# Optimization experiments

Hardware: AMD Instinct MI355X
Metric: run time of the kernel (lower is better)

## Reference

```python
import jax, jax.numpy as jnp
import numpy as np


def setup_inputs() -> dict:
    key = jax.random.key(0)
    ka, kb = jax.random.split(key)
    a = jax.random.normal(ka, (16384, 3), dtype=jnp.float32)
    b = jax.random.normal(kb, (16384, 3), dtype=jnp.float32)
    return {"a": a, "b": b}


def reference(a, b):
    # Pairwise Euclidean distances via ||a||^2 + ||b||^2 - 2 a.b (avoids [N,M,D] diff tensor).
    a2 = jnp.sum(a * a, axis=-1)            # [N]
    b2 = jnp.sum(b * b, axis=-1)            # [M]
    sq = a2[:, None] + b2[None, :] - 2.0 * jnp.einsum("nd,md->nm", a, b)  # [N,M]
    dist = jnp.sqrt(jnp.maximum(sq, 0.0))
    min_a = jnp.min(dist, axis=1)           # nearest b for each a
    min_b = jnp.min(dist, axis=0)           # nearest a for each b
    return jnp.mean(jnp.concatenate([min_a, min_b]))
```

## Files before the change

### kernel.cpp

```cpp
#include <hip/hip_runtime.h>

typedef unsigned int uint32;
typedef unsigned short ushort16;
typedef __attribute__((ext_vector_type(16))) float f32x16;
typedef __attribute__((ext_vector_type(8)))  short short8;

#define THREADS 256
#define FR 2
#define QB 256
#define JS 8
#define RB 128

__device__ inline ushort16 bf16rn(float x) {
    uint32 u = __float_as_uint(x);
    u += 0x7FFFu + ((u >> 16) & 1u);
    return (ushort16)(u >> 16);
}
__device__ inline float bf2f(ushort16 h) { return __uint_as_float(((uint32)h) << 16); }

__device__ inline void prep_one(const float* __restrict__ P, int np, int i,
                                short8* __restrict__ Qf, short8* __restrict__ Sf,
                                float* __restrict__ a2)
{
    ushort16 qs[16], ss[16];
#pragma unroll
    for (int s = 0; s < 16; ++s) { qs[s] = 0; ss[s] = 0; }
    float w = 0.f;
    if (i < np) {
        float c[3] = {P[3*i], P[3*i+1], P[3*i+2]};
        w = fmaf(c[0], c[0], fmaf(c[1], c[1], c[2]*c[2]));
#pragma unroll
        for (int cc = 0; cc < 3; ++cc) {
            ushort16 h = bf16rn(c[cc]);
            ushort16 m = bf16rn(c[cc] - bf2f(h));
            float bv = -2.f * c[cc];
            ushort16 bh = bf16rn(bv);
            ushort16 bm = bf16rn(bv - bf2f(bh));
            const int b = 4*cc;
            qs[b]=h;  qs[b+1]=h;  qs[b+2]=m;  qs[b+3]=m;
            ss[b]=bh; ss[b+1]=bm; ss[b+2]=bh; ss[b+3]=bm;
        }
        qs[12]=0x3F80; qs[13]=0x3F80; qs[14]=0x3F80;
        ushort16 wh = bf16rn(w);
        float r1 = w - bf2f(wh);
        ushort16 wm = bf16rn(r1);
        ushort16 wl = bf16rn(r1 - bf2f(wm));
        ss[12]=wh; ss[13]=wm; ss[14]=wl;
    } else {
        ss[12] = bf16rn(1e30f);
    }
    a2[i] = w;
    const int row = i & 31, grp = i >> 5;
#pragma unroll
    for (int h = 0; h < 2; ++h) {
        short8 qv, sv;
#pragma unroll
        for (int e = 0; e < 8; ++e) { qv[e] = (short)qs[8*h+e]; sv[e] = (short)ss[8*h+e]; }
        Qf[(size_t)grp*64 + h*32 + row] = qv;
        Sf[(size_t)grp*64 + h*32 + row] = sv;
    }
}

__global__ __launch_bounds__(THREADS) void cd_prep(
    const float* __restrict__ A, int n, int padN,
    const float* __restrict__ B, int m, int padM,
    short8* QfA, short8* SfA, float* a2A,
    short8* QfB, short8* SfB, float* a2B,
    uint32* bits)
{
    const int i = blockIdx.x * THREADS + threadIdx.x;
    if (i < n + m) bits[i] = 0x7F800000u;
    if (i < padN) prep_one(A, n, i, QfA, SfA, a2A);
    if (i < padM) prep_one(B, m, i, QfB, SfB, a2B);
}

__device__ inline float dppmin(float v, int ctrl) {
    float s;
    switch (ctrl) {
        case 0xB1:  s = __int_as_float(__builtin_amdgcn_mov_dpp(__float_as_int(v), 0xB1,  0xf, 0xf, false)); break;
        case 0x4E:  s = __int_as_float(__builtin_amdgcn_mov_dpp(__float_as_int(v), 0x4E,  0xf, 0xf, false)); break;
        case 0x141: s = __int_as_float(__builtin_amdgcn_mov_dpp(__float_as_int(v), 0x141, 0xf, 0xf, false)); break;
        default:    s = __int_as_float(__builtin_amdgcn_mov_dpp(__float_as_int(v), 0x140, 0xf, 0xf, false)); break;
    }
    return fminf(v, s);
}

__global__ __launch_bounds__(THREADS, 4) void cd_mfma(
    const short8* __restrict__ QfA, const short8* __restrict__ SfA,
    const float* __restrict__ a2A, int padN, int n,
    const short8* __restrict__ QfB, const short8* __restrict__ SfB,
    const float* __restrict__ a2B, int padM, int m,
    uint32* __restrict__ bits)
{
    const short8* Qf; const short8* Sf; const float* a2; uint32* outb;
    int nq, padQ, padS;
    if (blockIdx.z == 0) { Qf=QfA; a2=a2A; nq=n; padQ=padN; Sf=SfB; padS=padM; outb=bits;   }
    else                 { Qf=QfB; a2=a2B; nq=m; padQ=padM; Sf=SfA; padS=padN; outb=bits+n; }

    if ((int)(blockIdx.x * QB) >= padQ) return;
    const int ntiles = padS >> 5;
    const int tps = (ntiles + JS - 1) / JS;
    const int t0 = blockIdx.y * tps;
    const int t1 = min(t0 + tps, ntiles);
    if (t0 >= t1) return;

    const int tid = threadIdx.x, lane = tid & 63, wid = tid >> 6;
    const int qbase = blockIdx.x * QB + wid * (FR * 32);

    short8 av[FR];
#pragma unroll
    for (int f = 0; f < FR; ++f)
        av[f] = Qf[(size_t)((qbase >> 5) + f) * 64 + lane];

    float rmin[FR][16];
#pragma unroll
    for (int f = 0; f < FR; ++f)
#pragma unroll
        for (int r = 0; r < 16; ++r) rmin[f][r] = 1e30f;

    const f32x16 zero = {0.f,0.f,0.f,0.f,0.f,0.f,0.f,0.f,
                         0.f,0.f,0.f,0.f,0.f,0.f,0.f,0.f};

    const short8* Sl = Sf + (size_t)t0 * 64 + lane;
    const int nt = t1 - t0;

    short8 c0 = Sl[0];
    short8 c1 = (nt > 1) ? Sl[64] : c0;

    int it = 0;
    for (; it + 2 <= nt; it += 2) {
        const short8 b0 = c0, b1 = c1;
        const int nx = it + 2;
        if (nx < nt)     c0 = Sl[(size_t)nx * 64];
        if (nx + 1 < nt) c1 = Sl[(size_t)(nx + 1) * 64];
#pragma unroll
        for (int f = 0; f < FR; ++f) {
            const f32x16 cA = __builtin_amdgcn_mfma_f32_32x32x16_bf16(av[f], b0, zero, 0, 0, 0);
            const f32x16 cB = __builtin_amdgcn_mfma_f32_32x32x16_bf16(av[f], b1, zero, 0, 0, 0);
#pragma unroll
            for (int r = 0; r < 16; ++r)
                rmin[f][r] = fminf(fminf(rmin[f][r], cA[r]), cB[r]);
        }
    }
    if (it < nt) {
#pragma unroll
        for (int f = 0; f < FR; ++f) {
            const f32x16 cA = __builtin_amdgcn_mfma_f32_32x32x16_bf16(av[f], c0, zero, 0, 0, 0);
#pragma unroll
            for (int r = 0; r < 16; ++r) rmin[f][r] = fminf(rmin[f][r], cA[r]);
        }
    }

#pragma unroll
    for (int f = 0; f < FR; ++f)
#pragma unroll
        for (int r = 0; r < 16; ++r) {
            float v = rmin[f][r];
            v = dppmin(v, 0xB1);
            v = dppmin(v, 0x4E);
            v = dppmin(v, 0x141);
            v = dppmin(v, 0x140);
            v = fminf(v, __shfl_xor(v, 16, 64));
            rmin[f][r] = v;
        }

    if ((lane & 31) == 0) {
        const int h4 = (lane >> 5) * 4;
#pragma unroll
        for (int f = 0; f < FR; ++f)
#pragma unroll
            for (int qq = 0; qq < 4; ++qq) {
                const int rowb = qbase + f*32 + 8*qq + h4;
                const float4 aa = *(const float4*)(a2 + rowb);
                const float av4[4] = {aa.x, aa.y, aa.z, aa.w};
#pragma unroll
                for (int e = 0; e < 4; ++e) {
                    const int qi = rowb + e;
                    if (qi < nq) {
                        const float sq = fmaxf(rmin[f][4*qq + e] + av4[e], 0.f);
                        atomicMin(&outb[qi], __float_as_uint(sq));
                    }
                }
            }
    }
}

__global__ __launch_bounds__(THREADS) void cd_reduce1(
    const uint32* __restrict__ bits, int count, double* __restrict__ partials)
{
    double s = 0.0;
    for (int i = blockIdx.x * THREADS + threadIdx.x; i < count; i += gridDim.x * THREADS)
        s += (double)sqrtf(__uint_as_float(bits[i]));
#pragma unroll
    for (int off = 32; off; off >>= 1) s += __shfl_down(s, off, 64);
    __shared__ double sw[4];
    const int lane = threadIdx.x & 63, wid = threadIdx.x >> 6;
    if (lane == 0) sw[wid] = s;
    __syncthreads();
    if (threadIdx.x == 0) partials[blockIdx.x] = sw[0] + sw[1] + sw[2] + sw[3];
}

__global__ __launch_bounds__(THREADS) void cd_reduce2(
    const double* __restrict__ partials, int nb, int total, float* __restrict__ out)
{
    double s = 0.0;
    for (int i = threadIdx.x; i < nb; i += THREADS) s += partials[i];
#pragma unroll
    for (int off = 32; off; off >>= 1) s += __shfl_down(s, off, 64);
    __shared__ double sw[4];
    const int lane = threadIdx.x & 63, wid = threadIdx.x >> 6;
    if (lane == 0) sw[wid] = s;
    __syncthreads();
    if (threadIdx.x == 0)
        out[0] = (float)((sw[0] + sw[1] + sw[2] + sw[3]) / (double)total);
}

extern "C" void kernel_launch(void* const* d_in, const int* in_sizes, int n_in,
                              void* d_out, int out_size, void* d_ws, size_t ws_size,
                              hipStream_t stream) {
    const float* a = (const float*)d_in[0];
    const float* b = (const float*)d_in[1];
    const int n = in_sizes[0] / 3;
    const int m = in_sizes[1] / 3;
    const int total = n + m;
    float* out = (float*)d_out;

    const int padN = (n + QB - 1) / QB * QB;
    const int padM = (m + QB - 1) / QB * QB;

    char* wp = (char*)d_ws;
    short8* QfA = (short8*)wp;   wp += (size_t)padN * 64;
    short8* SfA = (short8*)wp;   wp += (size_t)padN * 64;
    float*  a2A = (float*)wp;    wp += (size_t)padN * 4;
    short8* QfB = (short8*)wp;   wp += (size_t)padM * 64;
    short8* SfB = (short8*)wp;   wp += (size_t)padM * 64;
    float*  a2B = (float*)wp;    wp += (size_t)padM * 4;
    uint32* bits = (uint32*)wp;  wp += (size_t)total * 4;
    wp = (char*)(((size_t)wp + 255) & ~(size_t)255);
    double* partials = (double*)wp;

    const int prepElems = max(max(padN, padM), total);
    cd_prep<<<(prepElems + THREADS - 1) / THREADS, THREADS, 0, stream>>>(
        a, n, padN, b, m, padM, QfA, SfA, a2A, QfB, SfB, a2B, bits);

    const int gx = max(padN, padM) / QB;
    dim3 grid(gx, JS, 2);
    cd_mfma<<<grid, THREADS, 0, stream>>>(QfA, SfA, a2A, padN, n,
                                          QfB, SfB, a2B, padM, m, bits);

    cd_reduce1<<<RB, THREADS, 0, stream>>>(bits, total, partials);
    cd_reduce2<<<1, THREADS, 0, stream>>>(partials, RB, total, out);
}
```

Baseline: 46.26 us.

## Use one query fragment per wave with deeper prefetch and higher occupancy

Each wave now handles a single 32-row query fragment instead of two, the query block shrinks to match, and the launch bounds ask for 8 blocks per SM instead of 4. The 2-way unrolled loop becomes a single-MFMA loop with a 3-deep register prefetch of source tiles. This frees registers for higher occupancy and latency hiding. In exchange, each source tile loaded is reused for half as many MFMAs, so global/L2 traffic per FLOP doubles.

Result: slower. 79.95 us (+72.8%).

```diff
diff --git a/kernel.cpp b/kernel.cpp
--- a/kernel.cpp
+++ b/kernel.cpp
@@ -6,8 +6,7 @@
 typedef __attribute__((ext_vector_type(8)))  short short8;
 
 #define THREADS 256
-#define FR 2
-#define QB 256
+#define QB 128
 #define JS 8
 #define RB 128
 
@@ -85,7 +84,7 @@
     return fminf(v, s);
 }
 
-__global__ __launch_bounds__(THREADS, 4) void cd_mfma(
+__global__ __launch_bounds__(THREADS, 8) void cd_mfma(
     const short8* __restrict__ QfA, const short8* __restrict__ SfA,
     const float* __restrict__ a2A, int padN, int n,
     const short8* __restrict__ QfB, const short8* __restrict__ SfB,
@@ -105,83 +104,61 @@
     if (t0 >= t1) return;
 
     const int tid = threadIdx.x, lane = tid & 63, wid = tid >> 6;
-    const int qbase = blockIdx.x * QB + wid * (FR * 32);
-
-    short8 av[FR];
-#pragma unroll
-    for (int f = 0; f < FR; ++f)
-        av[f] = Qf[(size_t)((qbase >> 5) + f) * 64 + lane];
-
-    float rmin[FR][16];
-#pragma unroll
-    for (int f = 0; f < FR; ++f)
-#pragma unroll
-        for (int r = 0; r < 16; ++r) rmin[f][r] = 1e30f;
+    const int qbase = blockIdx.x * QB + wid * 32;
+
+    const short8 av = Qf[(size_t)(qbase >> 5) * 64 + lane];
+
+    float rmin[16];
+#pragma unroll
+    for (int r = 0; r < 16; ++r) rmin[r] = 1e30f;
 
     const f32x16 zero = {0.f,0.f,0.f,0.f,0.f,0.f,0.f,0.f,
                          0.f,0.f,0.f,0.f,0.f,0.f,0.f,0.f};
 
-    const short8* Sl = Sf + (size_t)t0 * 64 + lane;
     const int nt = t1 - t0;
-
-    short8 c0 = Sl[0];
-    short8 c1 = (nt > 1) ? Sl[64] : c0;
-
-    int it = 0;
-    for (; it + 2 <= nt; it += 2) {
-        const short8 b0 = c0, b1 = c1;
-        const int nx = it + 2;
-        if (nx < nt)     c0 = Sl[(size_t)nx * 64];
-        if (nx + 1 < nt) c1 = Sl[(size_t)(nx + 1) * 64];
-#pragma unroll
-        for (int f = 0; f < FR; ++f) {
-            const f32x16 cA = __builtin_amdgcn_mfma_f32_32x32x16_bf16(av[f], b0, zero, 0, 0, 0);
-            const f32x16 cB = __builtin_amdgcn_mfma_f32_32x32x16_bf16(av[f], b1, zero, 0, 0, 0);
-#pragma unroll
-            for (int r = 0; r < 16; ++r)
-                rmin[f][r] = fminf(fminf(rmin[f][r], cA[r]), cB[r]);
-        }
-    }
-    if (it < nt) {
-#pragma unroll
-        for (int f = 0; f < FR; ++f) {
-            const f32x16 cA = __builtin_amdgcn_mfma_f32_32x32x16_bf16(av[f], c0, zero, 0, 0, 0);
-#pragma unroll
-            for (int r = 0; r < 16; ++r) rmin[f][r] = fminf(rmin[f][r], cA[r]);
-        }
-    }
-
-#pragma unroll
-    for (int f = 0; f < FR; ++f)
-#pragma unroll
-        for (int r = 0; r < 16; ++r) {
-            float v = rmin[f][r];
-            v = dppmin(v, 0xB1);
-            v = dppmin(v, 0x4E);
-            v = dppmin(v, 0x141);
-            v = dppmin(v, 0x140);
-            v = fminf(v, __shfl_xor(v, 16, 64));
-            rmin[f][r] = v;
-        }
+    const short8* p = Sf + (size_t)t0 * 64 + lane;
+
+    short8 c0 = p[0];
+    short8 c1 = (nt > 1) ? p[64] : c0;
+    short8 c2 = (nt > 2) ? p[128] : c0;
+    p += 192;
+
+    for (int it = 0; it < nt; ++it) {
+        const short8 b = c0;
+        c0 = c1; c1 = c2;
+        if (it + 3 < nt) { c2 = p[0]; p += 64; }
+        const f32x16 c = __builtin_amdgcn_mfma_f32_32x32x16_bf16(av, b, zero, 0, 0, 0);
+#pragma unroll
+        for (int r = 0; r < 16; ++r) rmin[r] = fminf(rmin[r], c[r]);
+    }
+
+#pragma unroll
+    for (int r = 0; r < 16; ++r) {
+        float v = rmin[r];
+        v = dppmin(v, 0xB1);
+        v = dppmin(v, 0x4E);
+        v = dppmin(v, 0x141);
+        v = dppmin(v, 0x140);
+        v = fminf(v, __shfl_xor(v, 16, 64));
+        rmin[r] = v;
+    }
 
     if ((lane & 31) == 0) {
         const int h4 = (lane >> 5) * 4;
 #pragma unroll
-        for (int f = 0; f < FR; ++f)
-#pragma unroll
-            for (int qq = 0; qq < 4; ++qq) {
-                const int rowb = qbase + f*32 + 8*qq + h4;
-                const float4 aa = *(const float4*)(a2 + rowb);
-                const float av4[4] = {aa.x, aa.y, aa.z, aa.w};
-#pragma unroll
-                for (int e = 0; e < 4; ++e) {
-                    const int qi = rowb + e;
-                    if (qi < nq) {
-                        const float sq = fmaxf(rmin[f][4*qq + e] + av4[e], 0.f);
-                        atomicMin(&outb[qi], __float_as_uint(sq));
-                    }
+        for (int qq = 0; qq < 4; ++qq) {
+            const int rowb = qbase + 8*qq + h4;
+            const float4 aa = *(const float4*)(a2 + rowb);
+            const float av4[4] = {aa.x, aa.y, aa.z, aa.w};
+#pragma unroll
+            for (int e = 0; e < 4; ++e) {
+                const int qi = rowb + e;
+                if (qi < nq) {
+                    const float sq = fmaxf(rmin[4*qq + e] + av4[e], 0.f);
+                    atomicMin(&outb[qi], __float_as_uint(sq));
                 }
             }
+        }
     }
 }
 
```
